# Optimization experiments

Hardware: AMD Instinct MI355X
Metric: run time of the kernel (lower is better)

## Reference

```python
import jax, jax.numpy as jnp
import numpy as np

N = 100000   # nodes
E = 1600000  # edges
F_IN = 128   # node_features
H = 64       # hidden_features


def setup_inputs() -> dict:
    key = jax.random.key(0)
    ks = jax.random.split(key, 16)
    s = 0.05
    return {
        "x": jax.random.normal(ks[0], (N, F_IN), dtype=jnp.float32),
        "edge_index": jax.random.randint(ks[1], (2, E), 0, N, dtype=jnp.int64),
        "W1": jax.random.normal(ks[2], (H, F_IN), dtype=jnp.float32) * s,
        "b1": jnp.zeros((H,), dtype=jnp.float32),
        "W2": jax.random.normal(ks[3], (H, H), dtype=jnp.float32) * s,
        "b2": jnp.zeros((H,), dtype=jnp.float32),
        "Wk": jax.random.normal(ks[4], (H, H), dtype=jnp.float32) * s,
        "bk": jnp.zeros((H,), dtype=jnp.float32),
        "Wq": jax.random.normal(ks[5], (H, H), dtype=jnp.float32) * s,
        "bq": jnp.zeros((H,), dtype=jnp.float32),
        "Wv": jax.random.normal(ks[6], (H, H), dtype=jnp.float32) * s,
        "bv": jnp.zeros((H,), dtype=jnp.float32),
        "Ws": jax.random.normal(ks[7], (H, H), dtype=jnp.float32) * s,  # lin_skip, bias=False
        "b_gate": jnp.zeros((H,), dtype=jnp.float32),                   # conv bias param
        "Wsc": jax.random.normal(ks[8], (1, H), dtype=jnp.float32) * s,
        "bsc": jnp.zeros((1,), dtype=jnp.float32),
    }


def reference(x, edge_index, W1, b1, W2, b2, Wk, bk, Wq, bq, Wv, bv, Ws, b_gate, Wsc, bsc):
    # MLP front-end: Linear + ReLU + Linear
    h = jax.nn.relu(x @ W1.T + b1)
    h = h @ W2.T + b2                      # [N, H]

    # ResGatedGraphConv (sum aggregation, sigmoid gating)
    k = h @ Wk.T + bk                      # key on destination nodes
    q = h @ Wq.T + bq                      # query on source nodes
    v = h @ Wv.T + bv                      # value on source nodes

    src = edge_index[0]                    # j
    dst = edge_index[1]                    # i
    # message_ij = sigmoid(k_i + q_j) * v_j, scatter-add to destination i
    msg = jax.nn.sigmoid(k[dst] + q[src]) * v[src]   # [E, H]
    agg = jax.ops.segment_sum(msg, dst, num_segments=N)

    out = agg + h @ Ws.T + b_gate          # root skip (no bias) + conv bias

    # scorer head
    score = out @ Wsc.T + bsc              # [N, 1]
    return score
```

## Files before the change

### kernel.cpp

```cpp
#include <hip/hip_runtime.h>

#define HD  64
#define FIN 128

#define WS_W1H   0
#define WS_W1L   4096
#define WS_MALL  8192
#define WS_BK    14848
#define WS_BQ    14912
#define WS_BVW   14976
#define WS_BASE  15040
#define WS_K     15104

#define BSHIFT 7
#define BSIZE  128
#define CHUNK  3200
#define MAXNPB 512
#define CAP2   3072

#define C1f  3.9026344e-3f
#define C3f  (-7.67612e-8f)
#define C5f  1.2236660e-12f

typedef __attribute__((ext_vector_type(8))) short short8;
typedef __attribute__((ext_vector_type(4))) float f32x4;

__device__ __forceinline__ unsigned bf16rne(float f) {
    unsigned u = __float_as_uint(f);
    unsigned r = ((u >> 16) & 1u) + 0x7fffu;
    return (u + r) >> 16;
}
__device__ __forceinline__ float blo(unsigned u) { return __uint_as_float(u << 16); }
__device__ __forceinline__ float bhi(unsigned u) { return __uint_as_float(u & 0xffff0000u); }

__device__ __forceinline__ float grp4(unsigned ku, unsigned qu, unsigned va,
                                      unsigned vb, float p) {
    #pragma unroll
    for (int i = 0; i < 4; ++i) {
        float kf = (float)((ku >> (8 * i)) & 255u);
        float qf = (float)((qu >> (8 * i)) & 255u);
        unsigned vu = (i < 2) ? va : vb;
        float vf = (i & 1) ? bhi(vu) : blo(vu);
        float xx = kf + qf;
        xx = fminf(fmaxf(xx, 128.f), 384.f);
        float sv = xx - 256.f;
        float z = sv * sv;
        float w = fmaf(z, C5f, C3f);
        w = fmaf(z, w, C1f);
        p = fmaf(vf * sv, w, p);
        p = fmaf(vf, 0.5f, p);
    }
    return p;
}

__global__ void gnn_prep(const float* __restrict__ W1, const float* __restrict__ W2,
                         const float* __restrict__ b2,
                         const float* __restrict__ Wk, const float* __restrict__ bk,
                         const float* __restrict__ Wq, const float* __restrict__ bq,
                         const float* __restrict__ Wv, const float* __restrict__ bv,
                         const float* __restrict__ Wsm, const float* __restrict__ Wsc,
                         const float* __restrict__ bgate, const float* __restrict__ bsc,
                         float* __restrict__ ws) {
    __shared__ float w2s[4096];
    __shared__ float wxsT[65 * 64];
    int b = blockIdx.x, t = threadIdx.x;
    unsigned short* w1h  = (unsigned short*)(ws + WS_W1H);
    unsigned short* w1l  = (unsigned short*)(ws + WS_W1L);
    unsigned short* mall = (unsigned short*)(ws + WS_MALL);
    if (b == 0) {
        for (int idx = t; idx < HD * FIN; idx += blockDim.x) {
            float v = W1[idx];
            unsigned u = __float_as_uint(v);
            w1h[idx] = (unsigned short)(u >> 16);
            float rem = v - __uint_as_float(u & 0xffff0000u);
            w1l[idx] = (unsigned short)bf16rne(rem);
        }
    } else if (b <= 12) {
        int m = (b - 1) >> 2, qtr = (b - 1) & 3;
        const float* Wx = (m == 0) ? Wk : (m == 1) ? Wq : Wv;
        const float* bx = (m == 0) ? bk : (m == 1) ? bq : bv;
        int boffw = (m == 0) ? WS_BK : (m == 1) ? WS_BQ : WS_BVW;
        for (int i = t * 4; i < 4096; i += 1024)
            *(float4*)&w2s[i] = *(const float4*)&W2[i];
        for (int idx = t; idx < 4096; idx += 256) {
            int o = idx >> 6, c = idx & 63;
            wxsT[c * 65 + o] = Wx[idx];
        }
        __syncthreads();
        for (int idx = t; idx < 1024; idx += 256) {
            int a = qtr * 16 + (idx >> 6), o = idx & 63;
            float acc = 0.f;
            for (int c = 0; c < HD; ++c) acc += w2s[c * HD + a] * wxsT[c * 65 + o];
            if (m == 2) acc *= Wsc[o];
            mall[(m * 64 + o) * HD + a] = (unsigned short)bf16rne(acc);
        }
        if (qtr == 0 && t < HD) {
            float acc = bx[t];
            for (int c = 0; c < HD; ++c) acc += b2[c] * wxsT[c * 65 + t];
            if (m == 2) acc *= Wsc[t];
            ws[boffw + t] = acc;
        }
    } else {
        __shared__ float wsk[HD];
        if (t < HD) {
            float a = 0.f;
            for (int d = 0; d < HD; ++d) a += Wsm[d * HD + t] * Wsc[d];
            wsk[t] = a;
        }
        __syncthreads();
        if (t < HD) {
            float a = 0.f;
            for (int c = 0; c < HD; ++c) a += W2[c * HD + t] * wsk[c];
            mall[192 * HD + t] = (unsigned short)bf16rne(a);
        }
        for (int idx = t; idx < 15 * HD; idx += 256)
            mall[193 * HD + idx] = 0;
        if (t == 0) {
            float a = bsc[0];
            for (int d = 0; d < HD; ++d) a += bgate[d] * Wsc[d];
            float acc2 = 0.f;
            for (int c = 0; c < HD; ++c) {
                float wk2 = 0.f;
                for (int d = 0; d < HD; ++d) wk2 += Wsm[d * HD + c] * Wsc[d];
                acc2 += b2[c] * wk2;
            }
            ws[WS_BASE] = a + acc2;
        }
    }
}

__global__ __launch_bounds__(256, 3) void gnn_node(const float* __restrict__ x,
                                                   const float* __restrict__ b1,
                                                   const float* __restrict__ ws,
                                                   uint4* __restrict__ karr,
                                                   uint4* __restrict__ qv,
                                                   float* __restrict__ score, int N) {
    __shared__ __align__(16) char smem[32768];
    char* XHb = smem;
    char* XLb = smem + 16384;

    int tid = threadIdx.x;
    int l = tid & 63, w = tid >> 6;
    int nbase = blockIdx.x * 64;

    #pragma unroll
    for (int it = 0; it < 8; ++it) {
        int idx = it * 64 + l;
        int nl = 16 * w + (idx >> 5);
        int c4 = idx & 31;
        int node = min(nbase + nl, N - 1);
        float4 v = ((const float4*)x)[(size_t)node * 32 + c4];
        unsigned u0 = __float_as_uint(v.x), u1 = __float_as_uint(v.y);
        unsigned u2 = __float_as_uint(v.z), u3 = __float_as_uint(v.w);
        uint2 hx, lx;
        hx.x = (u0 >> 16) | (u1 & 0xffff0000u);
        hx.y = (u2 >> 16) | (u3 & 0xffff0000u);
        float r0 = v.x - __uint_as_float(u0 & 0xffff0000u);
        float r1 = v.y - __uint_as_float(u1 & 0xffff0000u);
        float r2 = v.z - __uint_as_float(u2 & 0xffff0000u);
        float r3 = v.w - __uint_as_float(u3 & 0xffff0000u);
        lx.x = bf16rne(r0) | (bf16rne(r1) << 16);
        lx.y = bf16rne(r2) | (bf16rne(r3) << 16);
        int bo = (nl * 256 + c4 * 8) ^ ((nl & 7) << 4);
        *(uint2*)(XHb + bo) = hx;
        *(uint2*)(XLb + bo) = lx;
    }
    __syncthreads();

    int rl = l & 15, kb = l >> 4;
    int rowA = 16 * w + rl;
    int swzA = (rowA & 7) << 4;

    const unsigned short* w1h = (const unsigned short*)(ws + WS_W1H);
    const unsigned short* w1l = (const unsigned short*)(ws + WS_W1L);
    f32x4 acc1[4];
    #pragma unroll
    for (int t = 0; t < 4; ++t) {
        float bv = b1[t * 16 + rl];
        acc1[t] = (f32x4){bv, bv, bv, bv};
    }
    #pragma unroll
    for (int s = 0; s < 4; ++s) {
        int abyte = (rowA * 256 + s * 64 + kb * 16) ^ swzA;
        short8 ah = *(const short8*)(XHb + abyte);
        short8 al = *(const short8*)(XLb + abyte);
        int koff = s * 32 + kb * 8;
        #pragma unroll
        for (int t = 0; t < 4; ++t) {
            int col = t * 16 + rl;
            short8 bh = *(const short8*)&w1h[col * FIN + koff];
            short8 bl = *(const short8*)&w1l[col * FIN + koff];
            acc1[t] = __builtin_amdgcn_mfma_f32_16x16x32_bf16(ah, bh, acc1[t], 0, 0, 0);
            acc1[t] = __builtin_amdgcn_mfma_f32_16x16x32_bf16(al, bh, acc1[t], 0, 0, 0);
            acc1[t] = __builtin_amdgcn_mfma_f32_16x16x32_bf16(ah, bl, acc1[t], 0, 0, 0);
        }
    }
    __syncthreads();

    int r0w = (l >> 4) * 4;
    #pragma unroll
    for (int t = 0; t < 4; ++t) {
        int col = t * 16 + rl;
        #pragma unroll
        for (int r = 0; r < 4; ++r) {
            int row = 16 * w + r0w + r;
            float v = fmaxf(acc1[t][r], 0.f);
            int hb = (row * 128 + col * 2) ^ ((row & 7) << 4);
            *(unsigned short*)(smem + hb) = (unsigned short)bf16rne(v);
        }
    }
    __syncthreads();

    const unsigned short* mall = (const unsigned short*)(ws + WS_MALL);
    const float* bK = ws + WS_BK;
    const float* bQ = ws + WS_BQ;
    const float* bV = ws + WS_BVW;
    float base = ws[WS_BASE];
    f32x4 acc2[13];
    #pragma unroll
    for (int t = 0; t < 4; ++t) {
        float v = bK[t * 16 + rl];
        acc2[t] = (f32x4){v, v, v, v};
    }
    #pragma unroll
    for (int t = 0; t < 4; ++t) {
        float v = bQ[t * 16 + rl];
        acc2[4 + t] = (f32x4){v, v, v, v};
    }
    #pragma unroll
    for (int t = 0; t < 4; ++t) {
        float v = bV[t * 16 + rl];
        acc2[8 + t] = (f32x4){v, v, v, v};
    }
    acc2[12] = (f32x4){0.f, 0.f, 0.f, 0.f};

    #pragma unroll
    for (int s = 0; s < 2; ++s) {
        int abyte = (rowA * 128 + (s * 32 + kb * 8) * 2) ^ swzA;
        short8 a = *(const short8*)(smem + abyte);
        int koff = s * 32 + kb * 8;
        #pragma unroll
        for (int t = 0; t < 13; ++t) {
            short8 b = *(const short8*)&mall[(t * 16 + rl) * HD + koff];
            acc2[t] = __builtin_amdgcn_mfma_f32_16x16x32_bf16(a, b, acc2[t], 0, 0, 0);
        }
    }

    char* Ku = smem + 16384;
    char* Qu = smem + 20480;
    char* VW = smem + 24576;
    #pragma unroll
    for (int t = 0; t < 4; ++t) {
        int col = t * 16 + rl;
        #pragma unroll
        for (int r = 0; r < 4; ++r) {
            int row = 16 * w + r0w + r;
            int ek = min(max(__float2int_rn(fmaf(acc2[t][r],     64.f, 128.f)), 0), 255);
            int eq = min(max(__float2int_rn(fmaf(acc2[4 + t][r], 64.f, 128.f)), 0), 255);
            Ku[row * 64 + col] = (char)ek;
            Qu[row * 64 + col] = (char)eq;
            *(unsigned short*)(VW + row * 128 + col * 2) =
                (unsigned short)bf16rne(acc2[8 + t][r]);
        }
    }
    if (rl == 0) {
        #pragma unroll
        for (int r = 0; r < 4; ++r) {
            int node = nbase + 16 * w + r0w + r;
            if (node < N) score[node] = base + acc2[12][r];
        }
    }
    __syncthreads();

    {
        int n = tid >> 2, p = tid & 3;
        int node = nbase + n;
        if (node < N)
            karr[(size_t)node * 4 + p] = *(const uint4*)(Ku + n * 64 + p * 16);
    }
    #pragma unroll
    for (int it = 0; it < 3; ++it) {
        int n = tid >> 2, p = (tid & 3) + it * 4;
        int node = nbase + n;
        const char* srcp = (p < 4) ? (Qu + n * 64 + p * 16)
                                   : (VW + n * 128 + (p - 4) * 16);
        if (node < N) qv[(size_t)node * 12 + p] = *(const uint4*)srcp;
    }
}

__global__ __launch_bounds__(256, 2) void gnn_part(const int* __restrict__ ei,
                                                   unsigned* __restrict__ ebuf,
                                                   int* __restrict__ dir,
                                                   int E, int NPB, int nbkt) {
    __shared__ unsigned spk[CHUNK];
    __shared__ unsigned short sbk[CHUNK];
    __shared__ int hist[1024], off[1024], curx[1024], part[256];
    int t = threadIdx.x, blk = blockIdx.x;
    int base = blk * CHUNK;
    int n = min(CHUNK, E - base);

    #pragma unroll
    for (int i = 0; i < 4; ++i) hist[t * 4 + i] = 0;
    __syncthreads();

    for (int i = t; i < n; i += 256) {
        int src = ei[base + i], dst = ei[E + base + i];
        spk[i] = (unsigned)src | ((unsigned)(dst & (BSIZE - 1)) << 17);
        int b = dst >> BSHIFT;
        sbk[i] = (unsigned short)b;
        atomicAdd(&hist[b], 1);
    }
    __syncthreads();

    int h0 = hist[4 * t], h1 = hist[4 * t + 1], h2 = hist[4 * t + 2], h3 = hist[4 * t + 3];
    int tot = h0 + h1 + h2 + h3;
    part[t] = tot;
    __syncthreads();
    for (int s = 1; s < 256; s <<= 1) {
        int v = (t >= s) ? part[t - s] : 0;
        __syncthreads();
        part[t] += v;
        __syncthreads();
    }
    int excl = part[t] - tot;
    off[4 * t] = excl;           curx[4 * t] = excl;
    off[4 * t + 1] = excl + h0;  curx[4 * t + 1] = excl + h0;
    off[4 * t + 2] = excl + h0 + h1;      curx[4 * t + 2] = excl + h0 + h1;
    off[4 * t + 3] = excl + h0 + h1 + h2; curx[4 * t + 3] = excl + h0 + h1 + h2;
    __syncthreads();

    for (int i = t; i < n; i += 256) {
        int r = atomicAdd(&curx[sbk[i]], 1);
        ebuf[base + r] = spk[i];
    }
    for (int bb = t; bb <= nbkt; bb += 256)
        dir[bb * NPB + blk] = base + off[bb];
}

__global__ __launch_bounds__(256, 4) void gnn_bsort(const unsigned* __restrict__ ebuf,
                                                    const int* __restrict__ dir,
                                                    unsigned* __restrict__ ebuf2,
                                                    int* __restrict__ dir2,
                                                    int NPB, int WINDIV) {
    __shared__ unsigned ebl[CAP2];
    __shared__ int rs[MAXNPB], tl[MAXNPB], pf[MAXNPB + 1], part[256];
    __shared__ int hw[8], woff[9], wcur[8];
    int tid = threadIdx.x, db = blockIdx.x;

    for (int i = tid; i < NPB; i += 256) {
        int s = dir[db * NPB + i];
        rs[i] = s;
        tl[i] = dir[(db + 1) * NPB + i] - s;
    }
    if (tid < 8) hw[tid] = 0;
    __syncthreads();

    int i0 = 2 * tid, i1 = 2 * tid + 1;
    int l0 = (i0 < NPB) ? tl[i0] : 0;
    int l1 = (i1 < NPB) ? tl[i1] : 0;
    part[tid] = l0 + l1;
    __syncthreads();
    for (int s = 1; s < 256; s <<= 1) {
        int v = (tid >= s) ? part[tid - s] : 0;
        __syncthreads();
        part[tid] += v;
        __syncthreads();
    }
    int excl = part[tid] - (l0 + l1);
    if (i0 <= NPB) pf[i0] = excl;
    if (i1 <= NPB) pf[i1] = excl + l0;
    if (tid == 255) pf[NPB] = part[255];
    __syncthreads();
    int cnt = min(pf[NPB], CAP2);

    for (int r = tid; r < NPB; r += 256) {
        int s = rs[r], o = pf[r], n = tl[r];
        for (int j = 0; j < n; ++j) {
            int d = o + j;
            if (d < CAP2) ebl[d] = ebuf[s + j];
        }
    }
    __syncthreads();

    for (int i = tid; i < cnt; i += 256) {
        int w = (int)((ebl[i] & 0x1FFFFu) / (unsigned)WINDIV);
        atomicAdd(&hw[min(w, 7)], 1);
    }
    __syncthreads();
    if (tid == 0) {
        int s = 0;
        #pragma unroll
        for (int w = 0; w < 8; ++w) { woff[w] = s; wcur[w] = s; s += hw[w]; }
        woff[8] = s;
    }
    __syncthreads();

    for (int i = tid; i < cnt; i += 256) {
        unsigned pk = ebl[i];
        int w = min((int)((pk & 0x1FFFFu) / (unsigned)WINDIV), 7);
        int r = atomicAdd(&wcur[w], 1);
        ebuf2[(size_t)db * CAP2 + r] = pk;
    }
    if (tid <= 8) dir2[db * 9 + tid] = woff[tid];
}

__global__ __launch_bounds__(256, 8) void gnn_edge(const unsigned* __restrict__ ebuf2,
                                                   const int* __restrict__ dir2,
                                                   const uint4* __restrict__ karr,
                                                   const uint4* __restrict__ qv,
                                                   float* __restrict__ partial, int N) {
    __shared__ float accumF[BSIZE];
    int tid = threadIdx.x;
    int win = blockIdx.x & 7, db = blockIdx.x >> 3;
    int s = dir2[db * 9 + win], e2 = dir2[db * 9 + win + 1];
    size_t base = (size_t)db * CAP2;

    if (tid < BSIZE) accumF[tid] = 0.f;
    __syncthreads();

    int q = tid >> 2, f = tid & 3;
    for (int i = s + q; i < e2; i += 64) {
        unsigned pk = ebuf2[base + i];
        int src = (int)(pk & 0x1FFFFu);
        int dl = (int)(pk >> 17) & (BSIZE - 1);
        int dst = (db << BSHIFT) + dl;
        uint4 ku = karr[(size_t)dst * 4 + f];
        uint4 qu = qv[(size_t)src * 12 + f];
        uint4 va = qv[(size_t)src * 12 + 4 + 2 * f];
        uint4 vb = qv[(size_t)src * 12 + 5 + 2 * f];
        float p = 0.f;
        p = grp4(ku.x, qu.x, va.x, va.y, p);
        p = grp4(ku.y, qu.y, va.z, va.w, p);
        p = grp4(ku.z, qu.z, vb.x, vb.y, p);
        p = grp4(ku.w, qu.w, vb.z, vb.w, p);
        p += __shfl_down(p, 2, 4);
        p += __shfl_down(p, 1, 4);
        if (f == 0) atomicAdd(&accumF[dl], p);
    }
    __syncthreads();
    if (tid < BSIZE) {
        int node = (db << BSHIFT) + tid;
        if (node < N) partial[(size_t)win * N + node] = accumF[tid];
    }
}

__global__ __launch_bounds__(256) void gnn_final(const float* __restrict__ partial,
                                                 float* __restrict__ score, int N) {
    int n = blockIdx.x * 256 + threadIdx.x;
    if (n < N) {
        float s = score[n];
        #pragma unroll
        for (int w = 0; w < 8; ++w) s += partial[(size_t)w * N + n];
        score[n] = s;
    }
}

extern "C" void kernel_launch(void* const* d_in, const int* in_sizes, int n_in,
                              void* d_out, int out_size, void* d_ws, size_t ws_size,
                              hipStream_t stream) {
    const float* x    = (const float*)d_in[0];
    const int*   ei   = (const int*)d_in[1];
    const float* W1   = (const float*)d_in[2];
    const float* b1   = (const float*)d_in[3];
    const float* W2   = (const float*)d_in[4];
    const float* b2   = (const float*)d_in[5];
    const float* Wk   = (const float*)d_in[6];
    const float* bk   = (const float*)d_in[7];
    const float* Wq   = (const float*)d_in[8];
    const float* bq   = (const float*)d_in[9];
    const float* Wv   = (const float*)d_in[10];
    const float* bv   = (const float*)d_in[11];
    const float* Wsm  = (const float*)d_in[12];
    const float* bgat = (const float*)d_in[13];
    const float* Wsc  = (const float*)d_in[14];
    const float* bsc  = (const float*)d_in[15];

    int N = in_sizes[0] / FIN;
    int E = in_sizes[1] / 2;

    float* ws      = (float*)d_ws;
    float* karr    = ws + WS_K;
    float* qvarr   = karr + (size_t)N * 16;
    unsigned* ebuf = (unsigned*)(qvarr + (size_t)N * 48);
    int nbkt = (N + BSIZE - 1) >> BSHIFT;
    int NPB  = (E + CHUNK - 1) / CHUNK;
    int* dir = (int*)(ebuf + (size_t)E);
    unsigned* ebuf2 = (unsigned*)(dir + (size_t)(nbkt + 1) * NPB);
    int* dir2 = (int*)(ebuf2 + (size_t)nbkt * CAP2);
    float* partial = (float*)ebuf;
    float* score = (float*)d_out;

    int NB = (N + 63) / 64;
    int WINDIV = (N + 7) / 8;

    gnn_prep<<<14, 256, 0, stream>>>(W1, W2, b2, Wk, bk, Wq, bq, Wv, bv,
                                     Wsm, Wsc, bgat, bsc, ws);
    gnn_part<<<NPB, 256, 0, stream>>>(ei, ebuf, dir, E, NPB, nbkt);
    gnn_bsort<<<nbkt, 256, 0, stream>>>(ebuf, dir, ebuf2, dir2, NPB, WINDIV);
    gnn_node<<<NB, 256, 0, stream>>>(x, b1, ws, (uint4*)karr, (uint4*)qvarr,
                                     score, N);
    gnn_edge<<<nbkt * 8, 256, 0, stream>>>(ebuf2, dir2, (const uint4*)karr,
                                           (const uint4*)qvarr, partial, N);
    gnn_final<<<(N + 255) / 256, 256, 0, stream>>>(partial, score, N);
}
```

Baseline: 283.3 us.

## Fuse node MLP and edge partition into one launch with register-prefetched x tiles

Merges the node-feature kernel and the edge bucket-partition kernel into a single launch. Block IDs below NBLK run the node path and the rest run the partition path, so two independent workloads share the GPU concurrently and one launch is removed. Each node block now handles two 64-node tiles and prefetches the next tile's x rows into registers while the current tile's MFMAs run. The trade-offs are higher register pressure, the launch bound moving from 3 to 4 blocks per CU, and partition blocks now sharing the 32KB smem layout.

```diff
diff --git a/kernel.cpp b/kernel.cpp
--- a/kernel.cpp
+++ b/kernel.cpp
@@ -17,6 +17,7 @@
 #define CHUNK  3200
 #define MAXNPB 512
 #define CAP2   3072
+#define TPB    2
 
 #define C1f  3.9026344e-3f
 #define C3f  (-7.67612e-8f)
@@ -129,212 +130,239 @@
     }
 }
 
-__global__ __launch_bounds__(256, 3) void gnn_node(const float* __restrict__ x,
-                                                   const float* __restrict__ b1,
-                                                   const float* __restrict__ ws,
-                                                   uint4* __restrict__ karr,
-                                                   uint4* __restrict__ qv,
-                                                   float* __restrict__ score, int N) {
+__global__ __launch_bounds__(256, 4) void gnn_nodepart(
+        const float* __restrict__ x, const float* __restrict__ b1,
+        const float* __restrict__ ws, uint4* __restrict__ karr,
+        uint4* __restrict__ qv, float* __restrict__ score, int N, int NBt,
+        int NBLK, const int* __restrict__ ei, unsigned* __restrict__ ebuf,
+        int* __restrict__ dir, int E, int NPB, int nbkt) {
     __shared__ __align__(16) char smem[32768];
+    int tid = threadIdx.x;
+    int bid = blockIdx.x;
+
+    if (bid >= NBLK) {
+        unsigned* spk = (unsigned*)smem;
+        unsigned short* sbk = (unsigned short*)(smem + 12800);
+        int* hist = (int*)(smem + 19200);
+        int* off  = (int*)(smem + 23296);
+        int* curx = (int*)(smem + 27392);
+        int* prt  = (int*)(smem + 31488);
+        int t = tid, blk = bid - NBLK;
+        int base = blk * CHUNK;
+        int n = min(CHUNK, E - base);
+
+        #pragma unroll
+        for (int i = 0; i < 4; ++i) hist[t * 4 + i] = 0;
+        __syncthreads();
+
+        for (int i = t; i < n; i += 256) {
+            int src = ei[base + i], dst = ei[E + base + i];
+            spk[i] = (unsigned)src | ((unsigned)(dst & (BSIZE - 1)) << 17);
+            int b = dst >> BSHIFT;
+            sbk[i] = (unsigned short)b;
+            atomicAdd(&hist[b], 1);
+        }
+        __syncthreads();
+
+        int h0 = hist[4 * t], h1 = hist[4 * t + 1];
+        int h2 = hist[4 * t + 2], h3 = hist[4 * t + 3];
+        int tot = h0 + h1 + h2 + h3;
+        prt[t] = tot;
+        __syncthreads();
+        for (int s = 1; s < 256; s <<= 1) {
+            int v = (t >= s) ? prt[t - s] : 0;
+            __syncthreads();
+            prt[t] += v;
+            __syncthreads();
+        }
+        int excl = prt[t] - tot;
+        off[4 * t] = excl;           curx[4 * t] = excl;
+        off[4 * t + 1] = excl + h0;  curx[4 * t + 1] = excl + h0;
+        off[4 * t + 2] = excl + h0 + h1;      curx[4 * t + 2] = excl + h0 + h1;
+        off[4 * t + 3] = excl + h0 + h1 + h2; curx[4 * t + 3] = excl + h0 + h1 + h2;
+        __syncthreads();
+
+        for (int i = t; i < n; i += 256) {
+            int r = atomicAdd(&curx[sbk[i]], 1);
+            ebuf[base + r] = spk[i];
+        }
+        for (int bb = t; bb <= nbkt; bb += 256)
+            dir[bb * NPB + blk] = base + off[bb];
+        return;
+    }
+
     char* XHb = smem;
     char* XLb = smem + 16384;
-
-    int tid = threadIdx.x;
     int l = tid & 63, w = tid >> 6;
-    int nbase = blockIdx.x * 64;
-
-    #pragma unroll
-    for (int it = 0; it < 8; ++it) {
-        int idx = it * 64 + l;
-        int nl = 16 * w + (idx >> 5);
-        int c4 = idx & 31;
-        int node = min(nbase + nl, N - 1);
-        float4 v = ((const float4*)x)[(size_t)node * 32 + c4];
-        unsigned u0 = __float_as_uint(v.x), u1 = __float_as_uint(v.y);
-        unsigned u2 = __float_as_uint(v.z), u3 = __float_as_uint(v.w);
-        uint2 hx, lx;
-        hx.x = (u0 >> 16) | (u1 & 0xffff0000u);
-        hx.y = (u2 >> 16) | (u3 & 0xffff0000u);
-        float r0 = v.x - __uint_as_float(u0 & 0xffff0000u);
-        float r1 = v.y - __uint_as_float(u1 & 0xffff0000u);
-        float r2 = v.z - __uint_as_float(u2 & 0xffff0000u);
-        float r3 = v.w - __uint_as_float(u3 & 0xffff0000u);
-        lx.x = bf16rne(r0) | (bf16rne(r1) << 16);
-        lx.y = bf16rne(r2) | (bf16rne(r3) << 16);
-        int bo = (nl * 256 + c4 * 8) ^ ((nl & 7) << 4);
-        *(uint2*)(XHb + bo) = hx;
-        *(uint2*)(XLb + bo) = lx;
-    }
-    __syncthreads();
-
     int rl = l & 15, kb = l >> 4;
     int rowA = 16 * w + rl;
     int swzA = (rowA & 7) << 4;
+    int r0w = (l >> 4) * 4;
 
     const unsigned short* w1h = (const unsigned short*)(ws + WS_W1H);
     const unsigned short* w1l = (const unsigned short*)(ws + WS_W1L);
-    f32x4 acc1[4];
-    #pragma unroll
-    for (int t = 0; t < 4; ++t) {
-        float bv = b1[t * 16 + rl];
-        acc1[t] = (f32x4){bv, bv, bv, bv};
-    }
-    #pragma unroll
-    for (int s = 0; s < 4; ++s) {
-        int abyte = (rowA * 256 + s * 64 + kb * 16) ^ swzA;
-        short8 ah = *(const short8*)(XHb + abyte);
-        short8 al = *(const short8*)(XLb + abyte);
-        int koff = s * 32 + kb * 8;
-        #pragma unroll
-        for (int t = 0; t < 4; ++t) {
-            int col = t * 16 + rl;
-            short8 bh = *(const short8*)&w1h[col * FIN + koff];
-            short8 bl = *(const short8*)&w1l[col * FIN + koff];
-            acc1[t] = __builtin_amdgcn_mfma_f32_16x16x32_bf16(ah, bh, acc1[t], 0, 0, 0);
-            acc1[t] = __builtin_amdgcn_mfma_f32_16x16x32_bf16(al, bh, acc1[t], 0, 0, 0);
-            acc1[t] = __builtin_amdgcn_mfma_f32_16x16x32_bf16(ah, bl, acc1[t], 0, 0, 0);
-        }
-    }
-    __syncthreads();
-
-    int r0w = (l >> 4) * 4;
-    #pragma unroll
-    for (int t = 0; t < 4; ++t) {
-        int col = t * 16 + rl;
-        #pragma unroll
-        for (int r = 0; r < 4; ++r) {
-            int row = 16 * w + r0w + r;
-            float v = fmaxf(acc1[t][r], 0.f);
-            int hb = (row * 128 + col * 2) ^ ((row & 7) << 4);
-            *(unsigned short*)(smem + hb) = (unsigned short)bf16rne(v);
-        }
-    }
-    __syncthreads();
-
     const unsigned short* mall = (const unsigned short*)(ws + WS_MALL);
     const float* bK = ws + WS_BK;
     const float* bQ = ws + WS_BQ;
     const float* bV = ws + WS_BVW;
-    float base = ws[WS_BASE];
-    f32x4 acc2[13];
-    #pragma unroll
-    for (int t = 0; t < 4; ++t) {
-        float v = bK[t * 16 + rl];
-        acc2[t] = (f32x4){v, v, v, v};
-    }
-    #pragma unroll
-    for (int t = 0; t < 4; ++t) {
-        float v = bQ[t * 16 + rl];
-        acc2[4 + t] = (f32x4){v, v, v, v};
-    }
-    #pragma unroll
-    for (int t = 0; t < 4; ++t) {
-        float v = bV[t * 16 + rl];
-        acc2[8 + t] = (f32x4){v, v, v, v};
-    }
-    acc2[12] = (f32x4){0.f, 0.f, 0.f, 0.f};
-
-    #pragma unroll
-    for (int s = 0; s < 2; ++s) {
-        int abyte = (rowA * 128 + (s * 32 + kb * 8) * 2) ^ swzA;
-        short8 a = *(const short8*)(smem + abyte);
-        int koff = s * 32 + kb * 8;
-        #pragma unroll
-        for (int t = 0; t < 13; ++t) {
-            short8 b = *(const short8*)&mall[(t * 16 + rl) * HD + koff];
-            acc2[t] = __builtin_amdgcn_mfma_f32_16x16x32_bf16(a, b, acc2[t], 0, 0, 0);
-        }
-    }
-
-    char* Ku = smem + 16384;
-    char* Qu = smem + 20480;
-    char* VW = smem + 24576;
-    #pragma unroll
-    for (int t = 0; t < 4; ++t) {
-        int col = t * 16 + rl;
-        #pragma unroll
-        for (int r = 0; r < 4; ++r) {
-            int row = 16 * w + r0w + r;
-            int ek = min(max(__float2int_rn(fmaf(acc2[t][r],     64.f, 128.f)), 0), 255);
-            int eq = min(max(__float2int_rn(fmaf(acc2[4 + t][r], 64.f, 128.f)), 0), 255);
-            Ku[row * 64 + col] = (char)ek;
-            Qu[row * 64 + col] = (char)eq;
-            *(unsigned short*)(VW + row * 128 + col * 2) =
-                (unsigned short)bf16rne(acc2[8 + t][r]);
-        }
-    }
-    if (rl == 0) {
-        #pragma unroll
-        for (int r = 0; r < 4; ++r) {
-            int node = nbase + 16 * w + r0w + r;
-            if (node < N) score[node] = base + acc2[12][r];
-        }
-    }
-    __syncthreads();
-
+
+    float4 xr[8];
     {
-        int n = tid >> 2, p = tid & 3;
-        int node = nbase + n;
-        if (node < N)
-            karr[(size_t)node * 4 + p] = *(const uint4*)(Ku + n * 64 + p * 16);
-    }
-    #pragma unroll
-    for (int it = 0; it < 3; ++it) {
-        int n = tid >> 2, p = (tid & 3) + it * 4;
-        int node = nbase + n;
-        const char* srcp = (p < 4) ? (Qu + n * 64 + p * 16)
-                                   : (VW + n * 128 + (p - 4) * 16);
-        if (node < N) qv[(size_t)node * 12 + p] = *(const uint4*)srcp;
-    }
-}
-
-__global__ __launch_bounds__(256, 2) void gnn_part(const int* __restrict__ ei,
-                                                   unsigned* __restrict__ ebuf,
-                                                   int* __restrict__ dir,
-                                                   int E, int NPB, int nbkt) {
-    __shared__ unsigned spk[CHUNK];
-    __shared__ unsigned short sbk[CHUNK];
-    __shared__ int hist[1024], off[1024], curx[1024], part[256];
-    int t = threadIdx.x, blk = blockIdx.x;
-    int base = blk * CHUNK;
-    int n = min(CHUNK, E - base);
-
-    #pragma unroll
-    for (int i = 0; i < 4; ++i) hist[t * 4 + i] = 0;
-    __syncthreads();
-
-    for (int i = t; i < n; i += 256) {
-        int src = ei[base + i], dst = ei[E + base + i];
-        spk[i] = (unsigned)src | ((unsigned)(dst & (BSIZE - 1)) << 17);
-        int b = dst >> BSHIFT;
-        sbk[i] = (unsigned short)b;
-        atomicAdd(&hist[b], 1);
-    }
-    __syncthreads();
-
-    int h0 = hist[4 * t], h1 = hist[4 * t + 1], h2 = hist[4 * t + 2], h3 = hist[4 * t + 3];
-    int tot = h0 + h1 + h2 + h3;
-    part[t] = tot;
-    __syncthreads();
-    for (int s = 1; s < 256; s <<= 1) {
-        int v = (t >= s) ? part[t - s] : 0;
-        __syncthreads();
-        part[t] += v;
-        __syncthreads();
-    }
-    int excl = part[t] - tot;
-    off[4 * t] = excl;           curx[4 * t] = excl;
-    off[4 * t + 1] = excl + h0;  curx[4 * t + 1] = excl + h0;
-    off[4 * t + 2] = excl + h0 + h1;      curx[4 * t + 2] = excl + h0 + h1;
-    off[4 * t + 3] = excl + h0 + h1 + h2; curx[4 * t + 3] = excl + h0 + h1 + h2;
-    __syncthreads();
-
-    for (int i = t; i < n; i += 256) {
-        int r = atomicAdd(&curx[sbk[i]], 1);
-        ebuf[base + r] = spk[i];
-    }
-    for (int bb = t; bb <= nbkt; bb += 256)
-        dir[bb * NPB + blk] = base + off[bb];
+        int nb0 = bid * TPB * 64;
+        #pragma unroll
+        for (int it = 0; it < 8; ++it) {
+            int nl = 16 * w + it * 2 + (l >> 5), c4 = l & 31;
+            int node = min(nb0 + nl, N - 1);
+            xr[it] = ((const float4*)x)[(size_t)node * 32 + c4];
+        }
+    }
+
+    for (int tt = 0; tt < TPB; ++tt) {
+        int tile = bid * TPB + tt;
+        if (tile >= NBt) break;
+        int nbase = tile * 64;
+
+        __syncthreads();
+        #pragma unroll
+        for (int it = 0; it < 8; ++it) {
+            float4 v = xr[it];
+            int nl = 16 * w + it * 2 + (l >> 5), c4 = l & 31;
+            unsigned u0 = __float_as_uint(v.x), u1 = __float_as_uint(v.y);
+            unsigned u2 = __float_as_uint(v.z), u3 = __float_as_uint(v.w);
+            uint2 hx, lx;
+            hx.x = (u0 >> 16) | (u1 & 0xffff0000u);
+            hx.y = (u2 >> 16) | (u3 & 0xffff0000u);
+            float r0 = v.x - __uint_as_float(u0 & 0xffff0000u);
+            float r1 = v.y - __uint_as_float(u1 & 0xffff0000u);
+            float r2 = v.z - __uint_as_float(u2 & 0xffff0000u);
+            float r3 = v.w - __uint_as_float(u3 & 0xffff0000u);
+            lx.x = bf16rne(r0) | (bf16rne(r1) << 16);
+            lx.y = bf16rne(r2) | (bf16rne(r3) << 16);
+            int bo = (nl * 256 + c4 * 8) ^ ((nl & 7) << 4);
+            *(uint2*)(XHb + bo) = hx;
+            *(uint2*)(XLb + bo) = lx;
+        }
+        __syncthreads();
+
+        if (tt + 1 < TPB && tile + 1 < NBt) {
+            int nb1 = (tile + 1) * 64;
+            #pragma unroll
+            for (int it = 0; it < 8; ++it) {
+                int nl = 16 * w + it * 2 + (l >> 5), c4 = l & 31;
+                int node = min(nb1 + nl, N - 1);
+                xr[it] = ((const float4*)x)[(size_t)node * 32 + c4];
+            }
+        }
+
+        f32x4 acc1[4];
+        #pragma unroll
+        for (int t = 0; t < 4; ++t) {
+            float bv = b1[t * 16 + rl];
+            acc1[t] = (f32x4){bv, bv, bv, bv};
+        }
+        #pragma unroll
+        for (int s = 0; s < 4; ++s) {
+            int abyte = (rowA * 256 + s * 64 + kb * 16) ^ swzA;
+            short8 ah = *(const short8*)(XHb + abyte);
+            short8 al = *(const short8*)(XLb + abyte);
+            int koff = s * 32 + kb * 8;
+            #pragma unroll
+            for (int t = 0; t < 4; ++t) {
+                int col = t * 16 + rl;
+                short8 bh = *(const short8*)&w1h[col * FIN + koff];
+                short8 bl = *(const short8*)&w1l[col * FIN + koff];
+                acc1[t] = __builtin_amdgcn_mfma_f32_16x16x32_bf16(ah, bh, acc1[t], 0, 0, 0);
+                acc1[t] = __builtin_amdgcn_mfma_f32_16x16x32_bf16(al, bh, acc1[t], 0, 0, 0);
+                acc1[t] = __builtin_amdgcn_mfma_f32_16x16x32_bf16(ah, bl, acc1[t], 0, 0, 0);
+            }
+        }
+        __syncthreads();
+
+        #pragma unroll
+        for (int t = 0; t < 4; ++t) {
+            int col = t * 16 + rl;
+            #pragma unroll
+            for (int r = 0; r < 4; ++r) {
+                int row = 16 * w + r0w + r;
+                float v = fmaxf(acc1[t][r], 0.f);
+                int hb = (row * 128 + col * 2) ^ ((row & 7) << 4);
+                *(unsigned short*)(smem + hb) = (unsigned short)bf16rne(v);
+            }
+        }
+        __syncthreads();
+
+        float base = ws[WS_BASE];
+        f32x4 acc2[13];
+        #pragma unroll
+        for (int t = 0; t < 4; ++t) {
+            float v = bK[t * 16 + rl];
+            acc2[t] = (f32x4){v, v, v, v};
+        }
+        #pragma unroll
+        for (int t = 0; t < 4; ++t) {
+            float v = bQ[t * 16 + rl];
+            acc2[4 + t] = (f32x4){v, v, v, v};
+        }
+        #pragma unroll
+        for (int t = 0; t < 4; ++t) {
+            float v = bV[t * 16 + rl];
+            acc2[8 + t] = (f32x4){v, v, v, v};
+        }
+        acc2[12] = (f32x4){0.f, 0.f, 0.f, 0.f};
+
+        #pragma unroll
+        for (int s = 0; s < 2; ++s) {
+            int abyte = (rowA * 128 + (s * 32 + kb * 8) * 2) ^ swzA;
+            short8 a = *(const short8*)(smem + abyte);
+            int koff = s * 32 + kb * 8;
+            #pragma unroll
+            for (int t = 0; t < 13; ++t) {
+                short8 b = *(const short8*)&mall[(t * 16 + rl) * HD + koff];
+                acc2[t] = __builtin_amdgcn_mfma_f32_16x16x32_bf16(a, b, acc2[t], 0, 0, 0);
+            }
+        }
+
+        char* Ku = smem + 16384;
+        char* Qu = smem + 20480;
+        char* VW = smem + 24576;
+        #pragma unroll
+        for (int t = 0; t < 4; ++t) {
+            int col = t * 16 + rl;
+            #pragma unroll
+            for (int r = 0; r < 4; ++r) {
+                int row = 16 * w + r0w + r;
+                int ek = min(max(__float2int_rn(fmaf(acc2[t][r],     64.f, 128.f)), 0), 255);
+                int eq = min(max(__float2int_rn(fmaf(acc2[4 + t][r], 64.f, 128.f)), 0), 255);
+                Ku[row * 64 + col] = (char)ek;
+                Qu[row * 64 + col] = (char)eq;
+                *(unsigned short*)(VW + row * 128 + col * 2) =
+                    (unsigned short)bf16rne(acc2[8 + t][r]);
+            }
+        }
+        if (rl == 0) {
+            #pragma unroll
+            for (int r = 0; r < 4; ++r) {
+                int node = nbase + 16 * w + r0w + r;
+                if (node < N) score[node] = base + acc2[12][r];
+            }
+        }
+        __syncthreads();
+
+        {
+            int n = tid >> 2, p = tid & 3;
+            int node = nbase + n;
+            if (node < N)
+                karr[(size_t)node * 4 + p] = *(const uint4*)(Ku + n * 64 + p * 16);
+        }
+        #pragma unroll
+        for (int it = 0; it < 3; ++it) {
+            int n = tid >> 2, p = (tid & 3) + it * 4;
+            int node = nbase + n;
+            const char* srcp = (p < 4) ? (Qu + n * 64 + p * 16)
+                                       : (VW + n * 128 + (p - 4) * 16);
+            if (node < N) qv[(size_t)node * 12 + p] = *(const uint4*)srcp;
+        }
+    }
 }
 
 __global__ __launch_bounds__(256, 4) void gnn_bsort(const unsigned* __restrict__ ebuf,
@@ -490,15 +518,16 @@
     float* partial = (float*)ebuf;
     float* score = (float*)d_out;
 
-    int NB = (N + 63) / 64;
+    int NBt  = (N + 63) / 64;
+    int NBLK = (NBt + TPB - 1) / TPB;
     int WINDIV = (N + 7) / 8;
 
     gnn_prep<<<14, 256, 0, stream>>>(W1, W2, b2, Wk, bk, Wq, bq, Wv, bv,
                                      Wsm, Wsc, bgat, bsc, ws);
-    gnn_part<<<NPB, 256, 0, stream>>>(ei, ebuf, dir, E, NPB, nbkt);
+    gnn_nodepart<<<NBLK + NPB, 256, 0, stream>>>(x, b1, ws, (uint4*)karr,
+                                                 (uint4*)qvarr, score, N, NBt,
+                                                 NBLK, ei, ebuf, dir, E, NPB, nbkt);
     gnn_bsort<<<nbkt, 256, 0, stream>>>(ebuf, dir, ebuf2, dir2, NPB, WINDIV);
-    gnn_node<<<NB, 256, 0, stream>>>(x, b1, ws, (uint4*)karr, (uint4*)qvarr,
-                                     score, N);
     gnn_edge<<<nbkt * 8, 256, 0, stream>>>(ebuf2, dir2, (const uint4*)karr,
                                            (const uint4*)qvarr, partial, N);
     gnn_final<<<(N + 255) / 256, 256, 0, stream>>>(partial, score, N);
```

Result: slower. 352.3 us (+24.4%).
